# Performance work log

Hardware: AMD Instinct MI355X
Metric: run time of the kernel (lower is better)

The kernel has to match this reference:

```python
import jax, jax.numpy as jnp
import numpy as np

MESH = 128
ALPHA, KL, KS = 0.2, 0.3, 1.0

# 8 trilinear (CIC) corner offsets, shape (8, 3)
_OFFSETS = jnp.array([[i, j, k] for i in (0, 1) for j in (0, 1) for k in (0, 1)], dtype=jnp.int32)


def _cic_corners_weights(pos, mesh):
    """pos: [N,3] in grid units -> corners [N,8,3] int32, weights [N,8]."""
    i0 = jnp.floor(pos)
    frac = pos - i0                                    # [N,3]
    i0 = i0.astype(jnp.int32)
    corners = (i0[:, None, :] + _OFFSETS[None]) % mesh  # periodic wrap, [N,8,3]
    w = jnp.where(_OFFSETS[None] == 1, frac[:, None, :], 1.0 - frac[:, None, :])
    return corners, w.prod(-1)                          # [N,8,3], [N,8]


def cic_paint(pos, mesh):
    """Particle-to-mesh scatter (CIC deposit) onto a mesh^3 grid."""
    corners, w = _cic_corners_weights(pos, mesh)
    grid = jnp.zeros((mesh, mesh, mesh), dtype=pos.dtype)
    return grid.at[corners[..., 0], corners[..., 1], corners[..., 2]].add(w)


def cic_read(grid, pos):
    """Mesh-to-particle gather (CIC interpolation). grid: [M,M,M] -> [N]."""
    mesh = grid.shape[0]
    corners, w = _cic_corners_weights(pos, mesh)
    vals = grid[corners[..., 0], corners[..., 1], corners[..., 2]]  # [N,8]
    return (vals * w).sum(-1)


def fftk(mesh):
    """Angular wavenumber vectors broadcastable to the mesh^3 grid."""
    k = (2.0 * jnp.pi * jnp.fft.fftfreq(mesh)).astype(jnp.float32)
    return [k.reshape(mesh, 1, 1), k.reshape(1, mesh, 1), k.reshape(1, 1, mesh)]


def setup_inputs() -> dict:
    key = jax.random.key(0)
    k1, k2 = jax.random.split(key)
    n = MESH ** 3
    pos = jax.random.uniform(k1, (n, 3), dtype=jnp.float32) * MESH  # grid units
    vel = jax.random.normal(k2, (n, 3), dtype=jnp.float32)
    return {"pos": pos, "vel": vel, "full_drift_factor": jnp.ones((), dtype=jnp.float32)}


def reference(pos, vel, full_drift_factor):
    # 1. CIC paint -> density mesh
    delta = cic_paint(pos, MESH)
    # 2. 3D FFT
    delta_k = jnp.fft.fftn(delta)
    kvec = fftk(MESH)
    kk = kvec[0] ** 2 + kvec[1] ** 2 + kvec[2] ** 2
    kk_safe = jnp.where(kk == 0, 1.0, kk)
    # 3. PGD band-pass filter (zeroed at k=0)
    kl2, ks4 = KL ** 2, KS ** 4
    pgd_range = jnp.exp(-kl2 / kk_safe) * jnp.exp(-(kk ** 2) / ks4)
    pgd_range = jnp.where(kk == 0, 0.0, pgd_range)
    # inverse Laplacian kernel: -1/k^2, zero at k=0
    inv_lap = -jnp.where(kk == 0, 0.0, 1.0 / kk_safe)
    pot_k = delta_k * inv_lap * pgd_range
    # 4. three gradient IFFTs + CIC read-out at particle positions
    forces = jnp.stack(
        [cic_read(jnp.fft.ifftn(-1j * kvec[i] * pot_k).real.astype(pos.dtype), pos) for i in range(3)],
        axis=-1,
    )  # [N,3]
    v_pgd = (forces * ALPHA) / full_drift_factor
    vel_boosted = vel + v_pgd
    return (pos, vel_boosted)
```

## Files before the change

kernel.cpp:

```cpp
#include <hip/hip_runtime.h>

#define MESH  128
#define MESH2 16384
#define MESH3 2097152
#define NPART MESH3
#define TILE  16
#define LDP   (TILE + 1)
#define CAP   6
#define BSTRIDE 1536
typedef unsigned int u32;
typedef unsigned short u16;
typedef unsigned long long u64;

__device__ __forceinline__ float2 cmul(float2 a, float2 b) {
    return make_float2(a.x * b.x - a.y * b.y, a.x * b.y + a.y * b.x);
}
__device__ __forceinline__ float2 cadd(float2 a, float2 b) {
    return make_float2(a.x + b.x, a.y + b.y);
}
__device__ __forceinline__ float2 csub(float2 a, float2 b) {
    return make_float2(a.x - b.x, a.y - b.y);
}
__device__ __forceinline__ u16 f2bf(float x) {
    u32 b = __float_as_uint(x);
    return (u16)((b + 0x7FFFu + ((b >> 16) & 1u)) >> 16);
}
__device__ __forceinline__ float bf2f(u16 h) {
    return __uint_as_float(((u32)h) << 16);
}

__device__ __forceinline__ void fft128_fwd_lds(float2 (*__restrict__ s)[LDP],
                                               const float2* __restrict__ tw,
                                               int l, int bb) {
    #pragma unroll
    for (int pr = 0; pr < 3; ++pr) {
        const int st = 2 * pr;
        const int logq = 5 - st;
        const int q = 1 << logq;
        const int j = bb & (q - 1);
        const int g = bb >> logq;
        const int i0 = (g << (logq + 2)) + j;
        const float2 x0 = s[i0][l], x1 = s[i0 + q][l];
        const float2 x2 = s[i0 + 2 * q][l], x3 = s[i0 + 3 * q][l];
        const int m = j << st;
        const float2 wA = tw[m], wA2 = tw[m + 32], wB = tw[2 * m];
        const float2 u0 = cadd(x0, x2), u2 = cmul(csub(x0, x2), wA);
        const float2 u1 = cadd(x1, x3), u3 = cmul(csub(x1, x3), wA2);
        s[i0][l]         = cadd(u0, u1);
        s[i0 + q][l]     = cmul(csub(u0, u1), wB);
        s[i0 + 2 * q][l] = cadd(u2, u3);
        s[i0 + 3 * q][l] = cmul(csub(u2, u3), wB);
        __syncthreads();
    }
    #pragma unroll
    for (int itn = 0; itn < 2; ++itn) {
        const int i0 = (bb + (itn << 5)) << 1;
        const float2 x0 = s[i0][l], x1 = s[i0 + 1][l];
        s[i0][l]     = cadd(x0, x1);
        s[i0 + 1][l] = csub(x0, x1);
    }
}

__device__ __forceinline__ void fft128_inv_lds(float2 (*__restrict__ s)[LDP],
                                               const float2* __restrict__ tw,
                                               int l, int bb) {
    #pragma unroll
    for (int pr = 0; pr < 3; ++pr) {
        const int st = 2 * pr;
        const int p = 1 << st;
        const int j = bb & (p - 1);
        const int g = bb >> st;
        const int i0 = (g << (st + 2)) + j;
        const float2 wA = tw[j << (6 - st)];
        const int mB = j << (5 - st);
        const float2 wB = tw[mB], wB2 = tw[mB + 32];
        const float2 x0 = s[i0][l], x1 = s[i0 + p][l];
        const float2 x2 = s[i0 + 2 * p][l], x3 = s[i0 + 3 * p][l];
        const float2 a1 = cmul(x1, wA), a3 = cmul(x3, wA);
        const float2 u0 = cadd(x0, a1), u1 = csub(x0, a1);
        const float2 u2 = cadd(x2, a3), u3 = csub(x2, a3);
        const float2 b2 = cmul(u2, wB), b3 = cmul(u3, wB2);
        s[i0][l]         = cadd(u0, b2);
        s[i0 + p][l]     = cadd(u1, b3);
        s[i0 + 2 * p][l] = csub(u0, b2);
        s[i0 + 3 * p][l] = csub(u1, b3);
        __syncthreads();
    }
    #pragma unroll
    for (int itn = 0; itn < 2; ++itn) {
        const int b = bb + (itn << 5);
        const float2 w = tw[b];
        const float2 u = s[b][l];
        const float2 v = cmul(s[b + 64][l], w);
        s[b][l]      = cadd(u, v);
        s[b + 64][l] = csub(u, v);
    }
}

__device__ __forceinline__ void fft128_inv_lds_dual(float2 (*__restrict__ SA)[LDP],
                                                    float2 (*__restrict__ SB)[LDP],
                                                    const float2* __restrict__ tw,
                                                    int l, int bb) {
    #pragma unroll
    for (int pr = 0; pr < 3; ++pr) {
        const int st = 2 * pr;
        const int p = 1 << st;
        const int j = bb & (p - 1);
        const int g = bb >> st;
        const int i0 = (g << (st + 2)) + j;
        const float2 wA = tw[j << (6 - st)];
        const int mB = j << (5 - st);
        const float2 wB = tw[mB], wB2 = tw[mB + 32];
        {
            const float2 x0 = SA[i0][l], x1 = SA[i0 + p][l];
            const float2 x2 = SA[i0 + 2 * p][l], x3 = SA[i0 + 3 * p][l];
            const float2 a1 = cmul(x1, wA), a3 = cmul(x3, wA);
            const float2 u0 = cadd(x0, a1), u1 = csub(x0, a1);
            const float2 u2 = cadd(x2, a3), u3 = csub(x2, a3);
            const float2 b2 = cmul(u2, wB), b3 = cmul(u3, wB2);
            SA[i0][l]         = cadd(u0, b2);
            SA[i0 + p][l]     = cadd(u1, b3);
            SA[i0 + 2 * p][l] = csub(u0, b2);
            SA[i0 + 3 * p][l] = csub(u1, b3);
        }
        {
            const float2 x0 = SB[i0][l], x1 = SB[i0 + p][l];
            const float2 x2 = SB[i0 + 2 * p][l], x3 = SB[i0 + 3 * p][l];
            const float2 a1 = cmul(x1, wA), a3 = cmul(x3, wA);
            const float2 u0 = cadd(x0, a1), u1 = csub(x0, a1);
            const float2 u2 = cadd(x2, a3), u3 = csub(x2, a3);
            const float2 b2 = cmul(u2, wB), b3 = cmul(u3, wB2);
            SB[i0][l]         = cadd(u0, b2);
            SB[i0 + p][l]     = cadd(u1, b3);
            SB[i0 + 2 * p][l] = csub(u0, b2);
            SB[i0 + 3 * p][l] = csub(u1, b3);
        }
        __syncthreads();
    }
    #pragma unroll
    for (int itn = 0; itn < 2; ++itn) {
        const int b = bb + (itn << 5);
        const float2 w = tw[b];
        {
            const float2 u = SA[b][l];
            const float2 v = cmul(SA[b + 64][l], w);
            SA[b][l]      = cadd(u, v);
            SA[b + 64][l] = csub(u, v);
        }
        {
            const float2 u = SB[b][l];
            const float2 v = cmul(SB[b + 64][l], w);
            SB[b][l]      = cadd(u, v);
            SB[b + 64][l] = csub(u, v);
        }
    }
}

template <bool INV>
__device__ __forceinline__ void fft_y_body(float2* __restrict__ data, int bid, int t) {
    __shared__ float2 s[MESH][LDP];
    __shared__ float2 tw[64];
    if (t < 64) {
        float sv, cv;
        sincospif(-(float)t / 64.0f, &sv, &cv);
        tw[t] = make_float2(cv, INV ? -sv : sv);
    }
    const int outer = bid >> 3;
    const int z0 = (bid & 7) * TILE;
    const int base = outer * MESH2 + z0;
    for (int i = t; i < MESH * TILE; i += 512) {
        const int l = i & 15, e = i >> 4;
        s[e][l] = data[base + e * MESH + l];
    }
    __syncthreads();
    const int l  = t & 15;
    const int bb = t >> 4;
    if (!INV) fft128_fwd_lds(s, tw, l, bb);
    else      fft128_inv_lds(s, tw, l, bb);
    __syncthreads();
    for (int i = t; i < MESH * TILE; i += 512) {
        const int l2 = i & 15, e = i >> 4;
        data[base + e * MESH + l2] = s[e][l2];
    }
}

__global__ __launch_bounds__(512) void fft_y_fwd(float2* __restrict__ A) {
    fft_y_body<false>(A, blockIdx.x, threadIdx.x);
}
__global__ __launch_bounds__(512) void fft_y_inv_dual(float2* __restrict__ A,
                                                      float2* __restrict__ B) {
    float2* d = (blockIdx.x < 1024) ? A : B;
    fft_y_body<true>(d, blockIdx.x & 1023, threadIdx.x);
}

__global__ __launch_bounds__(512) void fft_z_fwd_merge(const float* __restrict__ ST,
                                                       float2* __restrict__ out) {
    __shared__ float2 s[MESH][LDP];
    __shared__ float2 tw[64];
    const int t = threadIdx.x;
    if (t < 64) {
        float sv, cv;
        sincospif(-(float)t / 64.0f, &sv, &cv);
        tw[t] = make_float2(cv, sv);
    }
    const int col0 = blockIdx.x * TILE;
    const int base = col0 * MESH;
    for (int i = t; i < MESH * TILE; i += 512) {
        const int lc = i >> 7;
        const int z  = i & 127;
        const int c  = col0 + lc;
        const int x = c >> 7, y = c & 127;
        const int tx = x >> 2, ty = y >> 1;
        const int hx = x & 3,  hy = y & 1;
        float v = ST[((tx << 6) | ty) * 1920 + ((hx * 3 + hy) << 7) + z];
        const int txm = (tx + 31) & 31;
        const int tym = (ty + 63) & 63;
        if (hx == 0)
            v += ST[((txm << 6) | ty) * 1920 + ((12 + hy) << 7) + z];
        if (hy == 0) {
            v += ST[((tx << 6) | tym) * 1920 + ((hx * 3 + 2) << 7) + z];
            if (hx == 0)
                v += ST[((txm << 6) | tym) * 1920 + (14 << 7) + z];
        }
        s[z][lc] = make_float2(v, 0.0f);
    }
    __syncthreads();
    const int l  = t & 15;
    const int bb = t >> 4;
    fft128_fwd_lds(s, tw, l, bb);
    __syncthreads();
    for (int i = t; i < MESH * TILE; i += 512)
        out[base + i] = s[i & 127][i >> 7];
}

__global__ __launch_bounds__(512) void fft_z_inv_dual(const float2* __restrict__ A,
                                                      const float2* __restrict__ B,
                                                      u32* __restrict__ Abf,
                                                      u16* __restrict__ Brl) {
    __shared__ float2 s[MESH][LDP];
    __shared__ float2 tw[64];
    const int t = threadIdx.x;
    if (t < 64) {
        float sv, cv;
        sincospif(-(float)t / 64.0f, &sv, &cv);
        tw[t] = make_float2(cv, -sv);
    }
    const bool isB = blockIdx.x >= 1024;
    const int base = (blockIdx.x & 1023) * (TILE * MESH);
    const float2* __restrict__ in = isB ? B : A;
    for (int i = t; i < MESH * TILE; i += 512)
        s[i & 127][i >> 7] = in[base + i];
    __syncthreads();
    const int l  = t & 15;
    const int bb = t >> 4;
    fft128_inv_lds(s, tw, l, bb);
    __syncthreads();
    if (isB) {
        for (int i = t; i < MESH * TILE; i += 512)
            Brl[base + i] = f2bf(s[i & 127][i >> 7].x);
    } else {
        for (int i = t; i < MESH * TILE; i += 512) {
            const float2 v = s[i & 127][i >> 7];
            Abf[base + i] = (u32)f2bf(v.x) | ((u32)f2bf(v.y) << 16);
        }
    }
}

__global__ __launch_bounds__(512) void fft_x_mega(float2* __restrict__ A,
                                                  float2* __restrict__ B) {
    __shared__ float2 SA[MESH][LDP];
    __shared__ float2 SB[MESH][LDP];
    __shared__ float2 twf[64];
    __shared__ float2 twi[64];
    const int t = threadIdx.x;
    if (t < 64) {
        float sv, cv;
        sincospif(-(float)t / 64.0f, &sv, &cv);
        twf[t] = make_float2(cv, sv);
        twi[t] = make_float2(cv, -sv);
    }
    const int cy = blockIdx.x >> 3;
    const int z0 = (blockIdx.x & 7) * TILE;
    const int base = cy * MESH + z0;

    for (int i = t; i < MESH * TILE; i += 512) {
        const int l = i & 15, e = i >> 4;
        SA[e][l] = A[base + e * MESH2 + l];
    }
    __syncthreads();

    const int l  = t & 15;
    const int bb = t >> 4;
    fft128_fwd_lds(SA, twf, l, bb);
    __syncthreads();

    const int jy = (int)(__brev((unsigned)cy) >> 25);
    const float c = 6.28318530717958647692f / 128.0f;
    const float ky = c * (float)(jy < 64 ? jy : jy - 128);
    for (int i = t; i < MESH * TILE; i += 512) {
        const int e = i & 127, ll = i >> 7;
        const int jx = (int)(__brev((unsigned)e) >> 25);
        const int jz = (int)(__brev((unsigned)(z0 + ll)) >> 25);
        const float kx = c * (float)(jx < 64 ? jx : jx - 128);
        const float kz = c * (float)(jz < 64 ? jz : jz - 128);
        const float kk = kx * kx + ky * ky + kz * kz;
        float2 a = SA[e][ll];
        float2 av = make_float2(0.f, 0.f), bv = make_float2(0.f, 0.f);
        if (kk > 0.0f) {
            const float inv_kk = 1.0f / kk;
            const float rng = __expf(-0.09f * inv_kk - kk * kk);
            const float sc  = -inv_kk * rng * (1.0f / 2097152.0f);
            const float pr = a.x * sc, pi = a.y * sc;
            av = make_float2(ky * pr + kx * pi, ky * pi - kx * pr);
            bv = make_float2(kz * pi, -kz * pr);
        }
        SA[e][ll] = av;
        SB[e][ll] = bv;
    }
    __syncthreads();

    fft128_inv_lds_dual(SA, SB, twi, l, bb);
    __syncthreads();

    for (int i = t; i < MESH * TILE; i += 512) {
        const int l2 = i & 15, e = i >> 4;
        A[base + e * MESH2 + l2] = SA[e][l2];
        B[base + e * MESH2 + l2] = SB[e][l2];
    }
}


__device__ __forceinline__ int bucket_of(float px, float py) {
    const int ix = ((int)floorf(px)) & 127;
    const int iy = ((int)floorf(py)) & 127;
    return ((ix >> 2) << 6) | (iy >> 1);
}

__device__ __forceinline__ u64 make_rec(float px, float py, float pz, int n) {
    const float fxx = floorf(px), fyy = floorf(py), fzz = floorf(pz);
    const int ix = ((int)fxx) & 127, iy = ((int)fyy) & 127, iz = ((int)fzz) & 127;
    const u32 qx = (u32)((px - fxx) * 1024.0f);
    const u32 qy = (u32)((py - fyy) * 1024.0f);
    const u32 qz = (u32)((pz - fzz) * 1024.0f);
    return (u64)iz | ((u64)(ix & 3) << 7) | ((u64)(iy & 1) << 9)
         | ((u64)qx << 11) | ((u64)qy << 21) | ((u64)qz << 31)
         | ((u64)(u32)n << 41);
}

__global__ __launch_bounds__(1024) void bin_kernel(const float* __restrict__ pos,
                                                   u32* __restrict__ gcnt,
                                                   u64* __restrict__ S,
                                                   float4* __restrict__ outp) {
    __shared__ u32 h[2048];
    const int t = threadIdx.x;
    for (int i = t; i < 2048; i += 1024) h[i] = 0;
    __syncthreads();
    const float4* pos4 = (const float4*)pos;
    const int base_q = blockIdx.x * 2048;
    float4 P[2][3];
    #pragma unroll
    for (int it = 0; it < 2; ++it) {
        const int q = base_q + (it << 10) + t;
        const float4 Pa = pos4[3 * q], Pb = pos4[3 * q + 1], Pc = pos4[3 * q + 2];
        P[it][0] = Pa; P[it][1] = Pb; P[it][2] = Pc;
        outp[3 * q]     = Pa;
        outp[3 * q + 1] = Pb;
        outp[3 * q + 2] = Pc;
        atomicAdd(&h[bucket_of(Pa.x, Pa.y)], 1u);
        atomicAdd(&h[bucket_of(Pa.w, Pb.x)], 1u);
        atomicAdd(&h[bucket_of(Pb.z, Pb.w)], 1u);
        atomicAdd(&h[bucket_of(Pc.y, Pc.z)], 1u);
    }
    __syncthreads();
    for (int i = t; i < 2048; i += 1024) {
        const u32 c = h[i];
        h[i] = c ? ((u32)i * BSTRIDE + atomicAdd(&gcnt[i], c)) : 0u;
    }
    __syncthreads();
    #pragma unroll
    for (int it = 0; it < 2; ++it) {
        const int q = base_q + (it << 10) + t;
        const int n = 4 * q;
        const float4 Pa = P[it][0], Pb = P[it][1], Pc = P[it][2];
        S[atomicAdd(&h[bucket_of(Pa.x, Pa.y)], 1u)] = make_rec(Pa.x, Pa.y, Pa.z, n);
        S[atomicAdd(&h[bucket_of(Pa.w, Pb.x)], 1u)] = make_rec(Pa.w, Pb.x, Pb.y, n + 1);
        S[atomicAdd(&h[bucket_of(Pb.z, Pb.w)], 1u)] = make_rec(Pb.z, Pb.w, Pc.x, n + 2);
        S[atomicAdd(&h[bucket_of(Pc.y, Pc.z)], 1u)] = make_rec(Pc.y, Pc.z, Pc.w, n + 3);
    }
}

__device__ __forceinline__ void decode(u64 v, int& iz, int& lx, int& ly,
                                       float& fx, float& fy, float& fz, int& n) {
    iz = (int)(v & 127);
    lx = (int)((v >> 7) & 3);
    ly = (int)((v >> 9) & 3);
    const float inv = 1.0f / 1024.0f;
    fx = (float)((v >> 11) & 1023) * inv;
    fy = (float)((v >> 21) & 1023) * inv;
    fz = (float)((v >> 31) & 1023) * inv;
    n = (int)((v >> 41) & 0x1FFFFF);
}

__global__ __launch_bounds__(512) void paint_kernel(const u64* __restrict__ S,
                                                    const u32* __restrict__ gcnt,
                                                    float* __restrict__ ST) {
    __shared__ u32 cnt[1024];
    __shared__ u32 rec[1024 * CAP];
    __shared__ u64 ovf[128];
    __shared__ u32 novf;
    const int t = threadIdx.x;
    for (int i = t; i < 1024; i += 512) cnt[i] = 0;
    if (t == 0) novf = 0;
    __syncthreads();
    const int b = blockIdx.x;
    const int start = b * BSTRIDE;
    const int end = start + (int)gcnt[b];
    for (int i = start + t; i < end; i += 512) {
        const u64 v = S[i];
        const int iz = (int)(v & 127);
        const int lx = (int)((v >> 7) & 3);
        const int ly = (int)((v >> 9) & 1);
        const int cell = (((lx << 1) | ly) << 7) | iz;
        const u32 r = (u32)((v >> 11) & 0x3FFFFFFFull);
        const u32 slot = atomicAdd(&cnt[cell], 1u);
        if (slot < CAP) rec[cell * CAP + slot] = r;
        else {
            const u32 o = atomicAdd(&novf, 1u);
            if (o < 128u) ovf[o] = ((u64)cell << 32) | r;
        }
    }
    __syncthreads();
    const u32 nv = novf > 128u ? 128u : novf;
    const float inv = 1.0f / 1024.0f;
    for (int i = t; i < 1920; i += 512) {
        const int hx = i / 384;
        const int hy = (i >> 7) % 3;
        const int z  = i & 127;
        float acc = 0.0f;
        #pragma unroll
        for (int sx = 0; sx < 2; ++sx) {
            const int bx = hx - 1 + sx;
            if ((unsigned)bx > 3u) continue;
            #pragma unroll
            for (int sy = 0; sy < 2; ++sy) {
                const int by = hy - 1 + sy;
                if ((unsigned)by > 1u) continue;
                #pragma unroll
                for (int sz = 0; sz < 2; ++sz) {
                    const int bz = (z - 1 + sz) & 127;
                    const int c = (((bx << 1) | by) << 7) | bz;
                    const int m = (int)min(cnt[c], (u32)CAP);
                    const int rb = c * CAP;
                    for (int k = 0; k < m; ++k) {
                        const u32 r = rec[rb + k];
                        const float fx = (float)(r & 1023) * inv;
                        const float fy = (float)((r >> 10) & 1023) * inv;
                        const float fz = (float)(r >> 20) * inv;
                        const float wx = sx ? (1.0f - fx) : fx;
                        const float wy = sy ? (1.0f - fy) : fy;
                        const float wz = sz ? (1.0f - fz) : fz;
                        acc += wx * wy * wz;
                    }
                }
            }
        }
        for (u32 j = 0; j < nv; ++j) {
            const u64 o = ovf[j];
            const int c = (int)(o >> 32);
            const int obx = (c >> 8) & 3, oby = (c >> 7) & 1, obz = c & 127;
            const int dx = hx - obx, dy = hy - oby, dz = (z - obz) & 127;
            if ((unsigned)dx < 2u && (unsigned)dy < 2u && dz < 2) {
                const u32 r = (u32)o;
                const float fx = (float)(r & 1023) * inv;
                const float fy = (float)((r >> 10) & 1023) * inv;
                const float fz = (float)(r >> 20) * inv;
                acc += (dx ? fx : 1.0f - fx) * (dy ? fy : 1.0f - fy)
                     * (dz ? fz : 1.0f - fz);
            }
        }
        ST[(size_t)b * 1920 + i] = acc;
    }
}

__global__ __launch_bounds__(512) void force_kernel(const u64* __restrict__ S,
                                                    const u32* __restrict__ gcnt,
                                                    const u32* __restrict__ Abf,
                                                    const u16* __restrict__ Brl,
                                                    u64* __restrict__ VP) {
    __shared__ float2 sxy[1920];
    __shared__ float  szz[1920];
    const int t = threadIdx.x;
    const int b = blockIdx.x;
    const int x0 = (b >> 6) << 2, y0 = (b & 63) << 1;
    for (int i = t; i < 1920; i += 512) {
        const int hx = i / 384;
        const int hy = (i >> 7) % 3;
        const int z = i & 127;
        const int g = (((x0 + hx) & 127) << 14) | (((y0 + hy) & 127) << 7) | z;
        const u32 ab = Abf[g];
        sxy[i] = make_float2(__uint_as_float(ab << 16),
                             __uint_as_float(ab & 0xFFFF0000u));
        szz[i] = bf2f(Brl[g]);
    }
    __syncthreads();
    const int start = b * BSTRIDE;
    const int end = start + (int)gcnt[b];
    for (int i = start + t; i < end; i += 512) {
        int iz, lx, ly, n;
        float fx, fy, fz;
        decode(S[i], iz, lx, ly, fx, fy, fz, n);
        const float wx[2] = {1.0f - fx, fx};
        const float wy[2] = {1.0f - fy, fy};
        const float wz[2] = {1.0f - fz, fz};
        float gx = 0.f, gy = 0.f, gz = 0.f;
        #pragma unroll
        for (int dx = 0; dx < 2; ++dx)
            #pragma unroll
            for (int dy = 0; dy < 2; ++dy) {
                const int bi = ((lx + dx) * 3 + (ly + dy)) << 7;
                const float wxy = wx[dx] * wy[dy];
                #pragma unroll
                for (int dz = 0; dz < 2; ++dz) {
                    const int idx2 = bi + ((iz + dz) & 127);
                    const float w = wxy * wz[dz];
                    const float2 a = sxy[idx2];
                    gx += w * a.x;
                    gy += w * a.y;
                    gz += w * szz[idx2];
                }
            }
        VP[n] = (u64)f2bf(gx) | ((u64)f2bf(gy) << 16) | ((u64)f2bf(gz) << 32);
    }
}

__global__ __launch_bounds__(256) void finalize_kernel(const float* __restrict__ vel,
                                                       const u64* __restrict__ VP,
                                                       const float* __restrict__ fdf,
                                                       float* __restrict__ out) {
    const int tid = blockIdx.x * 256 + threadIdx.x;
    const float sc = 0.2f / fdf[0];
    const float4* vel4 = (const float4*)vel;
    float4* outv = (float4*)out + (3 * NPART / 4);
    const float4 Va = vel4[3 * tid], Vb = vel4[3 * tid + 1], Vc = vel4[3 * tid + 2];
    const ulonglong2* VP2 = (const ulonglong2*)VP;
    const ulonglong2 qa = VP2[2 * tid];
    const ulonglong2 qb = VP2[2 * tid + 1];
    const u64 q[4] = {qa.x, qa.y, qb.x, qb.y};
    const float vv[12] = {Va.x, Va.y, Va.z, Va.w, Vb.x, Vb.y, Vb.z, Vb.w,
                          Vc.x, Vc.y, Vc.z, Vc.w};
    float ov[12];
    #pragma unroll
    for (int k = 0; k < 4; ++k) {
        const float gx = bf2f((u16)(q[k] & 0xFFFF));
        const float gy = bf2f((u16)((q[k] >> 16) & 0xFFFF));
        const float gz = bf2f((u16)((q[k] >> 32) & 0xFFFF));
        ov[3 * k]     = vv[3 * k]     + gx * sc;
        ov[3 * k + 1] = vv[3 * k + 1] + gy * sc;
        ov[3 * k + 2] = vv[3 * k + 2] + gz * sc;
    }
    outv[3 * tid]     = make_float4(ov[0], ov[1], ov[2], ov[3]);
    outv[3 * tid + 1] = make_float4(ov[4], ov[5], ov[6], ov[7]);
    outv[3 * tid + 2] = make_float4(ov[8], ov[9], ov[10], ov[11]);
}

extern "C" void kernel_launch(void* const* d_in, const int* in_sizes, int n_in,
                              void* d_out, int out_size, void* d_ws, size_t ws_size,
                              hipStream_t stream) {
    const float* pos = (const float*)d_in[0];
    const float* vel = (const float*)d_in[1];
    const float* fdf = (const float*)d_in[2];
    float* out = (float*)d_out;

    char* w = (char*)d_ws;
    float2* A   = (float2*)(w);
    float2* B   = (float2*)(w + ((size_t)1 << 24));
    float*  ST  = (float*)(w + ((size_t)2 << 24));
    u32*    Abf = (u32*)(w + ((size_t)3 << 24));
    u16*    Brl = (u16*)(w + ((size_t)3 << 24) + (size_t)MESH3 * 4);
    u64*    VP  = (u64*)(w + ((size_t)4 << 24));
    u64*    S   = (u64*)(w + ((size_t)5 << 24));
    u32*    gcnt = (u32*)(w + ((size_t)7 << 24));

    hipMemsetAsync(gcnt, 0, 2048 * sizeof(u32), stream);
    bin_kernel<<<256, 1024, 0, stream>>>(pos, gcnt, S, (float4*)out);

    paint_kernel<<<2048, 512, 0, stream>>>(S, gcnt, ST);

    fft_z_fwd_merge<<<1024, 512, 0, stream>>>(ST, A);
    fft_y_fwd<<<1024, 512, 0, stream>>>(A);
    fft_x_mega<<<1024, 512, 0, stream>>>(A, B);
    fft_y_inv_dual<<<2048, 512, 0, stream>>>(A, B);
    fft_z_inv_dual<<<2048, 512, 0, stream>>>(A, B, Abf, Brl);

    force_kernel<<<2048, 512, 0, stream>>>(S, gcnt, Abf, Brl, VP);
    finalize_kernel<<<2048, 256, 0, stream>>>(vel, VP, fdf, out);
}
```

Measured before the change: 255.4 us.

## Fuse inverse y and z FFT passes into one full-plane LDS kernel

Replaces the separate inverse y-FFT and inverse z-FFT kernels with a single kernel that loads a whole 128x128 plane per block into LDS and performs both 1D inverse FFTs before writing bf16 outputs. This removes one global read/write pass over both complex grids and a kernel launch. In exchange it uses large LDS per block and 1024-thread blocks, giving only 256 blocks and low occupancy.

```diff
diff --git a/kernel.cpp b/kernel.cpp
--- a/kernel.cpp
+++ b/kernel.cpp
@@ -6,6 +6,7 @@
 #define NPART MESH3
 #define TILE  16
 #define LDP   (TILE + 1)
+#define LDP2  129
 #define CAP   6
 #define BSTRIDE 1536
 typedef unsigned int u32;
@@ -58,42 +59,6 @@
         const float2 x0 = s[i0][l], x1 = s[i0 + 1][l];
         s[i0][l]     = cadd(x0, x1);
         s[i0 + 1][l] = csub(x0, x1);
-    }
-}
-
-__device__ __forceinline__ void fft128_inv_lds(float2 (*__restrict__ s)[LDP],
-                                               const float2* __restrict__ tw,
-                                               int l, int bb) {
-    #pragma unroll
-    for (int pr = 0; pr < 3; ++pr) {
-        const int st = 2 * pr;
-        const int p = 1 << st;
-        const int j = bb & (p - 1);
-        const int g = bb >> st;
-        const int i0 = (g << (st + 2)) + j;
-        const float2 wA = tw[j << (6 - st)];
-        const int mB = j << (5 - st);
-        const float2 wB = tw[mB], wB2 = tw[mB + 32];
-        const float2 x0 = s[i0][l], x1 = s[i0 + p][l];
-        const float2 x2 = s[i0 + 2 * p][l], x3 = s[i0 + 3 * p][l];
-        const float2 a1 = cmul(x1, wA), a3 = cmul(x3, wA);
-        const float2 u0 = cadd(x0, a1), u1 = csub(x0, a1);
-        const float2 u2 = cadd(x2, a3), u3 = csub(x2, a3);
-        const float2 b2 = cmul(u2, wB), b3 = cmul(u3, wB2);
-        s[i0][l]         = cadd(u0, b2);
-        s[i0 + p][l]     = cadd(u1, b3);
-        s[i0 + 2 * p][l] = csub(u0, b2);
-        s[i0 + 3 * p][l] = csub(u1, b3);
-        __syncthreads();
-    }
-    #pragma unroll
-    for (int itn = 0; itn < 2; ++itn) {
-        const int b = bb + (itn << 5);
-        const float2 w = tw[b];
-        const float2 u = s[b][l];
-        const float2 v = cmul(s[b + 64][l], w);
-        s[b][l]      = cadd(u, v);
-        s[b + 64][l] = csub(u, v);
     }
 }
 
@@ -156,17 +121,17 @@
     }
 }
 
-template <bool INV>
-__device__ __forceinline__ void fft_y_body(float2* __restrict__ data, int bid, int t) {
+__global__ __launch_bounds__(512) void fft_y_fwd(float2* __restrict__ data) {
     __shared__ float2 s[MESH][LDP];
     __shared__ float2 tw[64];
+    const int t = threadIdx.x;
     if (t < 64) {
         float sv, cv;
         sincospif(-(float)t / 64.0f, &sv, &cv);
-        tw[t] = make_float2(cv, INV ? -sv : sv);
-    }
-    const int outer = bid >> 3;
-    const int z0 = (bid & 7) * TILE;
+        tw[t] = make_float2(cv, sv);
+    }
+    const int outer = blockIdx.x >> 3;
+    const int z0 = (blockIdx.x & 7) * TILE;
     const int base = outer * MESH2 + z0;
     for (int i = t; i < MESH * TILE; i += 512) {
         const int l = i & 15, e = i >> 4;
@@ -175,22 +140,12 @@
     __syncthreads();
     const int l  = t & 15;
     const int bb = t >> 4;
-    if (!INV) fft128_fwd_lds(s, tw, l, bb);
-    else      fft128_inv_lds(s, tw, l, bb);
+    fft128_fwd_lds(s, tw, l, bb);
     __syncthreads();
     for (int i = t; i < MESH * TILE; i += 512) {
         const int l2 = i & 15, e = i >> 4;
         data[base + e * MESH + l2] = s[e][l2];
     }
-}
-
-__global__ __launch_bounds__(512) void fft_y_fwd(float2* __restrict__ A) {
-    fft_y_body<false>(A, blockIdx.x, threadIdx.x);
-}
-__global__ __launch_bounds__(512) void fft_y_inv_dual(float2* __restrict__ A,
-                                                      float2* __restrict__ B) {
-    float2* d = (blockIdx.x < 1024) ? A : B;
-    fft_y_body<true>(d, blockIdx.x & 1023, threadIdx.x);
 }
 
 __global__ __launch_bounds__(512) void fft_z_fwd_merge(const float* __restrict__ ST,
@@ -233,11 +188,11 @@
         out[base + i] = s[i & 127][i >> 7];
 }
 
-__global__ __launch_bounds__(512) void fft_z_inv_dual(const float2* __restrict__ A,
-                                                      const float2* __restrict__ B,
-                                                      u32* __restrict__ Abf,
-                                                      u16* __restrict__ Brl) {
-    __shared__ float2 s[MESH][LDP];
+__global__ __launch_bounds__(1024) void fft_yz_inv_mega(const float2* __restrict__ A,
+                                                        const float2* __restrict__ B,
+                                                        u32* __restrict__ Abf,
+                                                        u16* __restrict__ Brl) {
+    __shared__ float2 s[MESH][LDP2];
     __shared__ float2 tw[64];
     const int t = threadIdx.x;
     if (t < 64) {
@@ -245,23 +200,99 @@
         sincospif(-(float)t / 64.0f, &sv, &cv);
         tw[t] = make_float2(cv, -sv);
     }
-    const bool isB = blockIdx.x >= 1024;
-    const int base = (blockIdx.x & 1023) * (TILE * MESH);
+    const bool isB = blockIdx.x >= 128;
+    const int x = blockIdx.x & 127;
     const float2* __restrict__ in = isB ? B : A;
-    for (int i = t; i < MESH * TILE; i += 512)
-        s[i & 127][i >> 7] = in[base + i];
-    __syncthreads();
-    const int l  = t & 15;
-    const int bb = t >> 4;
-    fft128_inv_lds(s, tw, l, bb);
-    __syncthreads();
+    const int gbase = x * MESH2;
+    for (int i = t; i < MESH * MESH; i += 1024)
+        s[i >> 7][i & 127] = in[gbase + i];
+    __syncthreads();
+
+    const int col = t & 127;
+    const int wrk = t >> 7;
+
+    #pragma unroll
+    for (int pr = 0; pr < 3; ++pr) {
+        const int st = 2 * pr;
+        const int p = 1 << st;
+        #pragma unroll
+        for (int n = 0; n < 4; ++n) {
+            const int bb = wrk | (n << 3);
+            const int j = bb & (p - 1);
+            const int g = bb >> st;
+            const int i0 = (g << (st + 2)) + j;
+            const float2 wA = tw[j << (6 - st)];
+            const int mB = j << (5 - st);
+            const float2 wB = tw[mB], wB2 = tw[mB + 32];
+            const float2 x0 = s[i0][col], x1 = s[i0 + p][col];
+            const float2 x2 = s[i0 + 2 * p][col], x3 = s[i0 + 3 * p][col];
+            const float2 a1 = cmul(x1, wA), a3 = cmul(x3, wA);
+            const float2 u0 = cadd(x0, a1), u1 = csub(x0, a1);
+            const float2 u2 = cadd(x2, a3), u3 = csub(x2, a3);
+            const float2 b2 = cmul(u2, wB), b3 = cmul(u3, wB2);
+            s[i0][col]         = cadd(u0, b2);
+            s[i0 + p][col]     = cadd(u1, b3);
+            s[i0 + 2 * p][col] = csub(u0, b2);
+            s[i0 + 3 * p][col] = csub(u1, b3);
+        }
+        __syncthreads();
+    }
+    #pragma unroll
+    for (int n = 0; n < 8; ++n) {
+        const int b = wrk | (n << 3);
+        const float2 w = tw[b];
+        const float2 u = s[b][col];
+        const float2 v = cmul(s[b + 64][col], w);
+        s[b][col]      = cadd(u, v);
+        s[b + 64][col] = csub(u, v);
+    }
+    __syncthreads();
+
+    const int row = t & 127;
+    #pragma unroll
+    for (int pr = 0; pr < 3; ++pr) {
+        const int st = 2 * pr;
+        const int p = 1 << st;
+        #pragma unroll
+        for (int n = 0; n < 4; ++n) {
+            const int bb = wrk | (n << 3);
+            const int j = bb & (p - 1);
+            const int g = bb >> st;
+            const int i0 = (g << (st + 2)) + j;
+            const float2 wA = tw[j << (6 - st)];
+            const int mB = j << (5 - st);
+            const float2 wB = tw[mB], wB2 = tw[mB + 32];
+            const float2 x0 = s[row][i0], x1 = s[row][i0 + p];
+            const float2 x2 = s[row][i0 + 2 * p], x3 = s[row][i0 + 3 * p];
+            const float2 a1 = cmul(x1, wA), a3 = cmul(x3, wA);
+            const float2 u0 = cadd(x0, a1), u1 = csub(x0, a1);
+            const float2 u2 = cadd(x2, a3), u3 = csub(x2, a3);
+            const float2 b2 = cmul(u2, wB), b3 = cmul(u3, wB2);
+            s[row][i0]         = cadd(u0, b2);
+            s[row][i0 + p]     = cadd(u1, b3);
+            s[row][i0 + 2 * p] = csub(u0, b2);
+            s[row][i0 + 3 * p] = csub(u1, b3);
+        }
+        __syncthreads();
+    }
+    #pragma unroll
+    for (int n = 0; n < 8; ++n) {
+        const int b = wrk | (n << 3);
+        const float2 w = tw[b];
+        const float2 u = s[row][b];
+        const float2 v = cmul(s[row][b + 64], w);
+        s[row][b]      = cadd(u, v);
+        s[row][b + 64] = csub(u, v);
+    }
+    __syncthreads();
+
     if (isB) {
-        for (int i = t; i < MESH * TILE; i += 512)
-            Brl[base + i] = f2bf(s[i & 127][i >> 7].x);
+        for (int i = t; i < MESH * MESH; i += 1024)
+            Brl[gbase + i] = f2bf(s[i >> 7][i & 127].x);
     } else {
-        for (int i = t; i < MESH * TILE; i += 512) {
-            const float2 v = s[i & 127][i >> 7];
-            Abf[base + i] = (u32)f2bf(v.x) | ((u32)f2bf(v.y) << 16);
+        for (int i = t; i < MESH * MESH; i += 1024) {
+            const float2 v = s[i >> 7][i & 127];
+            Abf[gbase + i] = (u32)f2bf(v.x) | ((u32)f2bf(v.y) << 16);
         }
     }
 }
@@ -589,8 +620,7 @@
     fft_z_fwd_merge<<<1024, 512, 0, stream>>>(ST, A);
     fft_y_fwd<<<1024, 512, 0, stream>>>(A);
     fft_x_mega<<<1024, 512, 0, stream>>>(A, B);
-    fft_y_inv_dual<<<2048, 512, 0, stream>>>(A, B);
-    fft_z_inv_dual<<<2048, 512, 0, stream>>>(A, B, Abf, Brl);
+    fft_yz_inv_mega<<<256, 1024, 0, stream>>>(A, B, Abf, Brl);
 
     force_kernel<<<2048, 512, 0, stream>>>(S, gcnt, Abf, Brl, VP);
     finalize_kernel<<<2048, 256, 0, stream>>>(vel, VP, fdf, out);
```

New measurement: 249.3 us. 2.4% less time.
